# Performance work log

Measured on AMD Instinct MI355X. Metric: run time of the kernel, lower is better.

Reference implementation:

```python
import jax, jax.numpy as jnp
import numpy as np

S, B, I, H = 2048, 64, 256, 512


def setup_inputs() -> dict:
    key = jax.random.key(0)
    ks = jax.random.split(key, 13)
    f = lambda k, sh: jax.random.normal(k, sh, dtype=jnp.float32) * 0.05
    m = lambda k, sh: jax.random.randint(k, sh, 0, 2, dtype=jnp.int32)
    return {
        "x": f(ks[0], (S, B, I)),
        "W_ih0": f(ks[1], (H, I)),
        "W_hh0": f(ks[2], (H, H)),
        "b_ih0": f(ks[3], (H,)),
        "b_hh0": f(ks[4], (H,)),
        "W_ih1": f(ks[5], (H, H)),
        "W_hh1": f(ks[6], (H, H)),
        "b_ih1": f(ks[7], (H,)),
        "b_hh1": f(ks[8], (H,)),
        "mask_ih0": m(ks[9], (H, I)),
        "mask_hh0": m(ks[10], (H, H)),
        "mask_ih1": m(ks[11], (H, H)),
        "mask_hh1": m(ks[12], (H, H)),
    }


def _rnn_layer(x, Wih, Whh, bih, bhh):
    # x: [S, B, in]; tanh RNN layer, h0 = zeros. Precompute input projection
    # for all timesteps (one big GEMM), then scan the recurrence.
    xb = jnp.einsum('sbi,hi->sbh', x, Wih) + bih + bhh  # [S, B, H]

    def step(h, xt):
        h = jnp.tanh(xt + h @ Whh.T)
        return h, h

    h0 = jnp.zeros((x.shape[1], Whh.shape[0]), dtype=x.dtype)
    _, ys = jax.lax.scan(step, h0, xb)
    return ys  # [S, B, H]


def reference(x, W_ih0, W_hh0, b_ih0, b_hh0, W_ih1, W_hh1, b_ih1, b_hh1,
              mask_ih0, mask_hh0, mask_ih1, mask_hh1):
    dt = x.dtype
    y0 = _rnn_layer(x,
                    W_ih0 * mask_ih0.astype(dt), W_hh0 * mask_hh0.astype(dt),
                    b_ih0, b_hh0)
    y1 = _rnn_layer(y0,
                    W_ih1 * mask_ih1.astype(dt), W_hh1 * mask_hh1.astype(dt),
                    b_ih1, b_hh1)
    return y1[-1]  # last timestep hidden state: [B, H]
```

## Files before the change

### kernel.cpp

```cpp
#include <hip/hip_runtime.h>
#include <math.h>

typedef unsigned int u32;
typedef unsigned long long u64;
typedef unsigned short u16;
typedef __attribute__((ext_vector_type(8))) short short8;
typedef __attribute__((ext_vector_type(4))) float f4;
typedef __attribute__((ext_vector_type(4))) u32 u32x4;

#define Ssz 2048
#define Bsz 64
#define Isz 256
#define Hsz 512
#define KC0 24
#define KC1 32

#define WB0_OFF   0u
#define WB1_OFF   1572864u
#define BIAS0_OFF 3670016u
#define BIAS1_OFF 3672064u
#define FLAGS_OFF 3674112u
#define H0_OFF    3675136u
#define H1_OFF    4068352u

#define MFMA(a, b, c) __builtin_amdgcn_mfma_f32_16x16x32_bf16(a, b, c, 0, 0, 0)

__device__ __forceinline__ u16 f2bf(float f) {
  union { float f; u32 u; } v; v.f = f;
  u32 r = v.u + 0x7FFFu + ((v.u >> 16) & 1u);
  return (u16)(r >> 16);
}
__device__ __forceinline__ float bf2f(u16 h) {
  union { u32 u; float f; } v; v.u = ((u32)h) << 16;
  return v.f;
}
__device__ __forceinline__ u32 packbf(float f) {
  u16 hi = f2bf(f);
  u16 lo = f2bf(f - bf2f(hi));
  return (u32)hi | ((u32)lo << 16);
}
__device__ __forceinline__ void unpack2(u32 w0, u32 w1, u32& hi, u32& lo) {
  hi = __builtin_amdgcn_perm(w1, w0, 0x05040100u);
  lo = __builtin_amdgcn_perm(w1, w0, 0x07060302u);
}
__device__ __forceinline__ void cvt2(float a, float b, u32& hi, u32& lo) {
  u16 ha = f2bf(a), hb = f2bf(b);
  u16 la = f2bf(a - bf2f(ha)), lb = f2bf(b - bf2f(hb));
  hi = (u32)ha | ((u32)hb << 16);
  lo = (u32)la | ((u32)lb << 16);
}
__device__ __forceinline__ float ftanh(float xx) {
  float x = fminf(20.f, fmaxf(-20.f, xx));
  float e = __expf(2.f * x);
  return (e - 1.f) / (e + 1.f);
}

union frag { short8 s; u32 w[4]; };

__device__ __forceinline__ u64 ald64(const u64* p) {
  return __hip_atomic_load(p, __ATOMIC_RELAXED, __HIP_MEMORY_SCOPE_AGENT);
}
__device__ __forceinline__ u32 ald32(const u32* p) {
  return __hip_atomic_load(p, __ATOMIC_RELAXED, __HIP_MEMORY_SCOPE_AGENT);
}
__device__ __forceinline__ void ast32(u32* p, u32 v) {
  __hip_atomic_store(p, v, __ATOMIC_RELAXED, __HIP_MEMORY_SCOPE_AGENT);
}

__device__ __forceinline__ void spin_load(const u32* rb, int ks, int lane,
                                          u32 tag, u64 (&hb)[8][4]) {
  const u64 M = 0x0001000000010000ull;
  const u64 E = tag ? M : 0ull;
  while (1) {
    #pragma unroll
    for (int i = 0; i < 8; ++i) {
      const u64* pp = (const u64*)(rb + (2 * i + ks) * 512 + lane * 8);
      #pragma unroll
      for (int v = 0; v < 4; ++v) hb[i][v] = ald64(pp + v);
    }
    int ok = 1;
    #pragma unroll
    for (int i = 0; i < 8; ++i)
      #pragma unroll
      for (int v = 0; v < 4; ++v) ok &= (int)((hb[i][v] & M) == E);
    if (__all(ok)) break;
  }
}

__global__ void prep_weights(const float* __restrict__ Wih0, const float* __restrict__ Whh0,
                             const float* __restrict__ bih0, const float* __restrict__ bhh0,
                             const float* __restrict__ Wih1, const float* __restrict__ Whh1,
                             const float* __restrict__ bih1, const float* __restrict__ bhh1,
                             const int* __restrict__ mih0, const int* __restrict__ mhh0,
                             const int* __restrict__ mih1, const int* __restrict__ mhh1,
                             char* __restrict__ ws) {
  const int L0E = 768 * 512, L1E = 1024 * 512;
  const int TAGN = 3 * 32768;
  int e = blockIdx.x * blockDim.x + threadIdx.x;
  if (e >= L0E + L1E + 1024 + TAGN) return;
  if (e < L0E) {
    int f = e >> 9, fe = e & 511;
    int lane = fe >> 3, j = fe & 7;
    int n = lane & 15, q = lane >> 4;
    int nt = f / KC0, kc = f % KC0;
    int u = nt * 16 + n, k = kc * 32 + q * 8 + j;
    float w;
    if (k < 256) w = Wih0[u * 256 + k] * (float)mih0[u * 256 + k];
    else         w = Whh0[u * 512 + (k - 256)] * (float)mhh0[u * 512 + (k - 256)];
    ((u32*)(ws + WB0_OFF))[e] = packbf(w);
  } else if (e < L0E + L1E) {
    int e1 = e - L0E;
    int f = e1 >> 9, fe = e1 & 511;
    int lane = fe >> 3, j = fe & 7;
    int n = lane & 15, q = lane >> 4;
    int nt = f >> 5, kc = f & 31;
    int u = nt * 16 + n, k = kc * 32 + q * 8 + j;
    float w;
    if (k < 512) w = Wih1[u * 512 + k] * (float)mih1[u * 512 + k];
    else         w = Whh1[u * 512 + (k - 512)] * (float)mhh1[u * 512 + (k - 512)];
    ((u32*)(ws + WB1_OFF))[e1] = packbf(w);
  } else if (e < L0E + L1E + 1024) {
    int b2 = e - L0E - L1E;
    if (b2 < 512) ((float*)(ws + BIAS0_OFF))[b2] = bih0[b2] + bhh0[b2];
    else          ((float*)(ws + BIAS1_OFF))[b2 - 512] = bih1[b2 - 512] + bhh1[b2 - 512];
  } else {
    int ti = e - (L0E + L1E + 1024);
    u32* dst;
    if (ti < 32768)      dst = (u32*)(ws + H0_OFF) + ti;
    else if (ti < 65536) dst = (u32*)(ws + H0_OFF) + 32768 + ti;
    else                 dst = (u32*)(ws + H1_OFF) + (ti - 65536);
    *dst = 0x00010000u;
  }
}


__device__ __forceinline__ void run0(const float* __restrict__ x, char* __restrict__ ws,
                                     int m, int p, int tid, float (*red)[256]) {
  const int w = tid >> 6, lane = tid & 63, n = lane & 15, q = lane >> 4;
  const int nt = p * 4 + (w & 3), ks = w >> 2;
  const int b0 = m * 16;
  const u32* WB = (const u32*)(ws + WB0_OFF);
  u32* flags1 = (u32*)(ws + FLAGS_OFF + m * 256) + 16;
  const float bs = ((const float*)(ws + BIAS0_OFF))[nt * 16 + n];

  short8 Whi[12], Wlo[12];
  #pragma unroll
  for (int i = 0; i < 12; ++i) {
    const int kcg = 2 * i + ks;
    const u32* pw = WB + ((nt * KC0 + kcg) * 64 + lane) * 8;
    u32x4 a = *(const u32x4*)pw;
    u32x4 b = *(const u32x4*)(pw + 4);
    frag h, l;
    unpack2(a.x, a.y, h.w[0], l.w[0]);
    unpack2(a.z, a.w, h.w[1], l.w[1]);
    unpack2(b.x, b.y, h.w[2], l.w[2]);
    unpack2(b.z, b.w, h.w[3], l.w[3]);
    Whi[i] = h.s; Wlo[i] = l.s;
  }

  f4 xp[4][2];
  auto loadx = [&](int t) {
    #pragma unroll
    for (int i = 0; i < 4; ++i) {
      const int kcg = 2 * i + ks;
      const float* sx = x + ((long)t * Bsz + b0 + n) * Isz + kcg * 32 + q * 8;
      xp[i][0] = *(const f4*)sx;
      xp[i][1] = *(const f4*)(sx + 4);
    }
  };
  short8 Axh[4], Axl[4];
  auto cvtx = [&]() {
    #pragma unroll
    for (int i = 0; i < 4; ++i) {
      frag h, l;
      #pragma unroll
      for (int v = 0; v < 2; ++v) {
        f4 f = xp[i][v];
        cvt2(f.x, f.y, h.w[2 * v], l.w[2 * v]);
        cvt2(f.z, f.w, h.w[2 * v + 1], l.w[2 * v + 1]);
      }
      Axh[i] = h.s; Axl[i] = l.s;
    }
  };
  loadx(0); cvtx();

  const int cst = (nt * 16 + n) >> 5;
  const int qp = ((nt * 2) + (n >> 3)) & 3;
  const int jj = n & 7;
  int last1 = 0;

  for (int t = 0; t < Ssz; ++t) {
    f4 acc0 = {0.f, 0.f, 0.f, 0.f}, acc1 = {0.f, 0.f, 0.f, 0.f};
    #pragma unroll
    for (int i = 0; i < 4; ++i) {
      acc0 = MFMA(Axh[i], Whi[i], acc0);
      acc1 = MFMA(Axh[i], Wlo[i], acc1);
      acc0 = MFMA(Axl[i], Whi[i], acc0);
    }
    loadx(t + 1 < Ssz ? t + 1 : t);
    const u32* rb = (const u32*)(ws + H0_OFF) + (((t + 2) % 3) * 4 + m) * 8192;
    u64 hb[8][4];
    spin_load(rb, ks, lane, (u32)((t + 1) & 1), hb);
    #pragma unroll
    for (int i = 0; i < 8; ++i) {
      frag h, l;
      #pragma unroll
      for (int v = 0; v < 4; ++v)
        unpack2((u32)hb[i][v], (u32)(hb[i][v] >> 32), h.w[v], l.w[v]);
      acc0 = MFMA(h.s, Whi[4 + i], acc0);
      acc1 = MFMA(h.s, Wlo[4 + i], acc1);
      acc0 = MFMA(l.s, Whi[4 + i], acc0);
    }
    f4 acc = acc0 + acc1;
    if (tid == 0 && last1 < t - 2) {
      const int tgt = t - 2;
      while (1) {
        int mn = 0x7fffffff;
        #pragma unroll
        for (int i = 0; i < 8; ++i) { int f = (int)ald32(flags1 + i); if (f < mn) mn = f; }
        if (mn >= tgt) { last1 = mn; break; }
      }
    }
    *(f4*)&red[w][lane * 4] = acc;
    __syncthreads();
    if (w < 4) {
      u32* wb = (u32*)(ws + H0_OFF) + ((t % 3) * 4 + m) * 8192;
      const u32 tb = (u32)(t & 1) << 16;
      f4 s0 = *(f4*)&red[w][lane * 4];
      f4 s1 = *(f4*)&red[w + 4][lane * 4];
      #pragma unroll
      for (int r = 0; r < 4; ++r) {
        float val = ftanh(bs + s0[r] + s1[r]);
        u32 pv = (packbf(val) & 0xFFFEFFFFu) | tb;
        ast32(wb + cst * 512 + ((q * 4 + r) + 16 * qp) * 8 + jj, pv);
      }
    }
    __syncthreads();
    cvtx();
  }
}

__device__ __forceinline__ void run1(char* __restrict__ ws, float* __restrict__ out,
                                     int m, int p, int tid, float (*red)[256]) {
  const int w = tid >> 6, lane = tid & 63, n = lane & 15, q = lane >> 4;
  const int nt = p * 4 + (w & 3), ks = w >> 2;
  const int b0 = m * 16;
  const u32* WB = (const u32*)(ws + WB1_OFF);
  u32* flags1 = (u32*)(ws + FLAGS_OFF + m * 256) + 16;
  const float bs = ((const float*)(ws + BIAS1_OFF))[nt * 16 + n];

  short8 Whi[16], Wlo[16];
  #pragma unroll
  for (int i = 0; i < 16; ++i) {
    const int kcg = 2 * i + ks;
    const u32* pw = WB + ((nt * KC1 + kcg) * 64 + lane) * 8;
    u32x4 a = *(const u32x4*)pw;
    u32x4 b = *(const u32x4*)(pw + 4);
    frag h, l;
    unpack2(a.x, a.y, h.w[0], l.w[0]);
    unpack2(a.z, a.w, h.w[1], l.w[1]);
    unpack2(b.x, b.y, h.w[2], l.w[2]);
    unpack2(b.z, b.w, h.w[3], l.w[3]);
    Whi[i] = h.s; Wlo[i] = l.s;
  }

  const int cst = (nt * 16 + n) >> 5;
  const int qp = ((nt * 2) + (n >> 3)) & 3;
  const int jj = n & 7;

  for (int t = 1; t <= Ssz; ++t) {
    f4 acc0 = {0.f, 0.f, 0.f, 0.f}, acc1 = {0.f, 0.f, 0.f, 0.f};
    {
      const u32* rb = (const u32*)(ws + H0_OFF) + (((t - 1) % 3) * 4 + m) * 8192;
      u64 hb[8][4];
      spin_load(rb, ks, lane, (u32)((t - 1) & 1), hb);
      #pragma unroll
      for (int i = 0; i < 8; ++i) {
        frag h, l;
        #pragma unroll
        for (int v = 0; v < 4; ++v)
          unpack2((u32)hb[i][v], (u32)(hb[i][v] >> 32), h.w[v], l.w[v]);
        acc0 = MFMA(h.s, Whi[i], acc0);
        acc1 = MFMA(h.s, Wlo[i], acc1);
        acc0 = MFMA(l.s, Whi[i], acc0);
      }
    }
    {
      const u32* rb = (const u32*)(ws + H1_OFF) + ((t & 1) * 4 + m) * 8192;
      u64 hb[8][4];
      spin_load(rb, ks, lane, (u32)(((t - 1) >> 1) & 1), hb);
      #pragma unroll
      for (int i = 0; i < 8; ++i) {
        frag h, l;
        #pragma unroll
        for (int v = 0; v < 4; ++v)
          unpack2((u32)hb[i][v], (u32)(hb[i][v] >> 32), h.w[v], l.w[v]);
        acc0 = MFMA(h.s, Whi[8 + i], acc0);
        acc1 = MFMA(h.s, Wlo[8 + i], acc1);
        acc0 = MFMA(l.s, Whi[8 + i], acc0);
      }
    }
    f4 acc = acc0 + acc1;
    *(f4*)&red[w][lane * 4] = acc;
    __syncthreads();
    if (tid == 0) ast32(flags1 + p, (u32)t);
    if (w < 4) {
      u32* wb = (u32*)(ws + H1_OFF) + (((t - 1) & 1) * 4 + m) * 8192;
      const u32 tb = (u32)((t >> 1) & 1) << 16;
      f4 s0 = *(f4*)&red[w][lane * 4];
      f4 s1 = *(f4*)&red[w + 4][lane * 4];
      #pragma unroll
      for (int r = 0; r < 4; ++r) {
        float val = ftanh(bs + s0[r] + s1[r]);
        u32 pv = (packbf(val) & 0xFFFEFFFFu) | tb;
        ast32(wb + cst * 512 + ((q * 4 + r) + 16 * qp) * 8 + jj, pv);
        if (t == Ssz) out[(b0 + q * 4 + r) * Hsz + nt * 16 + n] = val;
      }
    }
    __syncthreads();
  }
}

__global__ __launch_bounds__(512, 2) void rnn_persist(const float* __restrict__ x,
                                                      char* __restrict__ ws,
                                                      float* __restrict__ out) {
  __shared__ float red[8][256];
  const int tid = threadIdx.x;
  const int wg = blockIdx.x;
  const int m = (wg >> 3) & 3, p = wg & 7;
  if (wg < 32) run0(x, ws, m, p, tid, red);
  else         run1(ws, out, m, p, tid, red);
}

extern "C" void kernel_launch(void* const* d_in, const int* in_sizes, int n_in,
                              void* d_out, int out_size, void* d_ws, size_t ws_size,
                              hipStream_t stream) {
  const float* x    = (const float*)d_in[0];
  const float* Wih0 = (const float*)d_in[1];
  const float* Whh0 = (const float*)d_in[2];
  const float* bih0 = (const float*)d_in[3];
  const float* bhh0 = (const float*)d_in[4];
  const float* Wih1 = (const float*)d_in[5];
  const float* Whh1 = (const float*)d_in[6];
  const float* bih1 = (const float*)d_in[7];
  const float* bhh1 = (const float*)d_in[8];
  const int* mih0   = (const int*)d_in[9];
  const int* mhh0   = (const int*)d_in[10];
  const int* mih1   = (const int*)d_in[11];
  const int* mhh1   = (const int*)d_in[12];
  char* ws = (char*)d_ws;

  hipMemsetAsync(ws + FLAGS_OFF, 0, 1024 + 393216 + 262144, stream);

  const int tot = 768 * 512 + 1024 * 512 + 1024 + 3 * 32768;
  prep_weights<<<(tot + 255) / 256, 256, 0, stream>>>(
      Wih0, Whh0, bih0, bhh0, Wih1, Whh1, bih1, bhh1,
      mih0, mhh0, mih1, mhh1, ws);

  rnn_persist<<<64, 512, 0, stream>>>(x, ws, (float*)d_out);
}
```

Measured before the change: 16.10 ms.

## Drop intra-block K-split reduction; one wave owns full K per tile with deeper ring

Each wave now computes a full 16-wide output tile over the whole K dimension, keeping all weight fragments in registers. This removes the shared-memory reduction and both __syncthreads per timestep, and blocks shrink to 256 threads. The hidden-state ring buffers deepen (5 slots for layer 0, 3 for layer 1), so layer 0 can run further ahead before waiting on per-wave layer-1 flags. Each wave also uses four independent MFMA accumulators to break the dependency chain. The cost is doubled register pressure per wave and serial spin loads of the full hidden state per wave, with half as many waves to hide latency.

```diff
diff --git a/kernel.cpp b/kernel.cpp
--- a/kernel.cpp
+++ b/kernel.cpp
@@ -14,6 +14,8 @@
 #define Hsz 512
 #define KC0 24
 #define KC1 32
+#define D0 5
+#define D1 3
 
 #define WB0_OFF   0u
 #define WB1_OFF   1572864u
@@ -21,7 +23,7 @@
 #define BIAS1_OFF 3672064u
 #define FLAGS_OFF 3674112u
 #define H0_OFF    3675136u
-#define H1_OFF    4068352u
+#define H1_OFF    4330496u
 
 #define MFMA(a, b, c) __builtin_amdgcn_mfma_f32_16x16x32_bf16(a, b, c, 0, 0, 0)
 
@@ -67,16 +69,16 @@
   __hip_atomic_store(p, v, __ATOMIC_RELAXED, __HIP_MEMORY_SCOPE_AGENT);
 }
 
-__device__ __forceinline__ void spin_load(const u32* rb, int ks, int lane,
-                                          u32 tag, u64 (&hb)[8][4]) {
+__device__ __forceinline__ void spin8(const u32* rb, int cbase, int lane,
+                                      u32 par, u64 (&hb)[8][4]) {
   const u64 M = 0x0001000000010000ull;
-  const u64 E = tag ? M : 0ull;
+  const u64 E = par ? M : 0ull;
+  const u64* base = (const u64*)(rb + cbase * 512 + lane * 8);
   while (1) {
     #pragma unroll
     for (int i = 0; i < 8; ++i) {
-      const u64* pp = (const u64*)(rb + (2 * i + ks) * 512 + lane * 8);
       #pragma unroll
-      for (int v = 0; v < 4; ++v) hb[i][v] = ald64(pp + v);
+      for (int v = 0; v < 4; ++v) hb[i][v] = ald64(base + i * 256 + v);
     }
     int ok = 1;
     #pragma unroll
@@ -86,6 +88,16 @@
     if (__all(ok)) break;
   }
 }
+
+#define HSTEP(ii, WH, WL) do { frag h_, l_;                                 \
+    unpack2((u32)hb[ii][0], (u32)(hb[ii][0] >> 32), h_.w[0], l_.w[0]);      \
+    unpack2((u32)hb[ii][1], (u32)(hb[ii][1] >> 32), h_.w[1], l_.w[1]);      \
+    unpack2((u32)hb[ii][2], (u32)(hb[ii][2] >> 32), h_.w[2], l_.w[2]);      \
+    unpack2((u32)hb[ii][3], (u32)(hb[ii][3] >> 32), h_.w[3], l_.w[3]);      \
+    c[(ii) & 3]       = MFMA(h_.s, WH, c[(ii) & 3]);                        \
+    c[((ii) + 1) & 3] = MFMA(h_.s, WL, c[((ii) + 1) & 3]);                  \
+    c[((ii) + 2) & 3] = MFMA(l_.s, WH, c[((ii) + 2) & 3]);                  \
+  } while (0)
 
 __global__ void prep_weights(const float* __restrict__ Wih0, const float* __restrict__ Whh0,
                              const float* __restrict__ bih0, const float* __restrict__ bhh0,
@@ -95,7 +107,7 @@
                              const int* __restrict__ mih1, const int* __restrict__ mhh1,
                              char* __restrict__ ws) {
   const int L0E = 768 * 512, L1E = 1024 * 512;
-  const int TAGN = 3 * 32768;
+  const int TAGN = 131072;
   int e = blockIdx.x * blockDim.x + threadIdx.x;
   if (e >= L0E + L1E + 1024 + TAGN) return;
   if (e < L0E) {
@@ -126,28 +138,29 @@
   } else {
     int ti = e - (L0E + L1E + 1024);
     u32* dst;
-    if (ti < 32768)      dst = (u32*)(ws + H0_OFF) + ti;
-    else if (ti < 65536) dst = (u32*)(ws + H0_OFF) + 32768 + ti;
-    else                 dst = (u32*)(ws + H1_OFF) + (ti - 65536);
+    if (ti < 98304) {
+      int s = ti >> 15;
+      dst = (u32*)(ws + H0_OFF) + (2 * s) * 32768 + (ti & 32767);
+    } else {
+      dst = (u32*)(ws + H1_OFF) + 2 * 32768 + (ti - 98304);
+    }
     *dst = 0x00010000u;
   }
 }
 
 
 __device__ __forceinline__ void run0(const float* __restrict__ x, char* __restrict__ ws,
-                                     int m, int p, int tid, float (*red)[256]) {
-  const int w = tid >> 6, lane = tid & 63, n = lane & 15, q = lane >> 4;
-  const int nt = p * 4 + (w & 3), ks = w >> 2;
+                                     int m, int nt, int lane) {
+  const int n = lane & 15, q = lane >> 4;
   const int b0 = m * 16;
   const u32* WB = (const u32*)(ws + WB0_OFF);
-  u32* flags1 = (u32*)(ws + FLAGS_OFF + m * 256) + 16;
   const float bs = ((const float*)(ws + BIAS0_OFF))[nt * 16 + n];
-
-  short8 Whi[12], Wlo[12];
+  const u32* fl = (const u32*)(ws + FLAGS_OFF) + m * 64;
+
+  short8 Whi[KC0], Wlo[KC0];
   #pragma unroll
-  for (int i = 0; i < 12; ++i) {
-    const int kcg = 2 * i + ks;
-    const u32* pw = WB + ((nt * KC0 + kcg) * 64 + lane) * 8;
+  for (int kc = 0; kc < KC0; ++kc) {
+    const u32* pw = WB + ((nt * KC0 + kc) * 64 + lane) * 8;
     u32x4 a = *(const u32x4*)pw;
     u32x4 b = *(const u32x4*)(pw + 4);
     frag h, l;
@@ -155,105 +168,87 @@
     unpack2(a.z, a.w, h.w[1], l.w[1]);
     unpack2(b.x, b.y, h.w[2], l.w[2]);
     unpack2(b.z, b.w, h.w[3], l.w[3]);
-    Whi[i] = h.s; Wlo[i] = l.s;
-  }
-
-  f4 xp[4][2];
+    Whi[kc] = h.s; Wlo[kc] = l.s;
+  }
+
+  f4 xp[8][2];
   auto loadx = [&](int t) {
     #pragma unroll
-    for (int i = 0; i < 4; ++i) {
-      const int kcg = 2 * i + ks;
-      const float* sx = x + ((long)t * Bsz + b0 + n) * Isz + kcg * 32 + q * 8;
+    for (int i = 0; i < 8; ++i) {
+      const float* sx = x + ((long)t * Bsz + b0 + n) * Isz + i * 32 + q * 8;
       xp[i][0] = *(const f4*)sx;
       xp[i][1] = *(const f4*)(sx + 4);
     }
   };
-  short8 Axh[4], Axl[4];
+  short8 Axh[8], Axl[8];
   auto cvtx = [&]() {
     #pragma unroll
-    for (int i = 0; i < 4; ++i) {
+    for (int i = 0; i < 8; ++i) {
       frag h, l;
-      #pragma unroll
-      for (int v = 0; v < 2; ++v) {
-        f4 f = xp[i][v];
-        cvt2(f.x, f.y, h.w[2 * v], l.w[2 * v]);
-        cvt2(f.z, f.w, h.w[2 * v + 1], l.w[2 * v + 1]);
-      }
+      cvt2(xp[i][0].x, xp[i][0].y, h.w[0], l.w[0]);
+      cvt2(xp[i][0].z, xp[i][0].w, h.w[1], l.w[1]);
+      cvt2(xp[i][1].x, xp[i][1].y, h.w[2], l.w[2]);
+      cvt2(xp[i][1].z, xp[i][1].w, h.w[3], l.w[3]);
       Axh[i] = h.s; Axl[i] = l.s;
     }
   };
   loadx(0); cvtx();
 
-  const int cst = (nt * 16 + n) >> 5;
-  const int qp = ((nt * 2) + (n >> 3)) & 3;
-  const int jj = n & 7;
-  int last1 = 0;
+  const int sbase = (nt >> 1) * 512 +
+                    (q * 4 + 16 * (((nt & 1) << 1) + (n >> 3))) * 8 + (n & 7);
+  int sR = D0 - 1, sW = 0, last1 = 0;
+  u64 hb[8][4];
 
   for (int t = 0; t < Ssz; ++t) {
-    f4 acc0 = {0.f, 0.f, 0.f, 0.f}, acc1 = {0.f, 0.f, 0.f, 0.f};
-    #pragma unroll
-    for (int i = 0; i < 4; ++i) {
-      acc0 = MFMA(Axh[i], Whi[i], acc0);
-      acc1 = MFMA(Axh[i], Wlo[i], acc1);
-      acc0 = MFMA(Axl[i], Whi[i], acc0);
+    f4 c[4] = {{0,0,0,0},{0,0,0,0},{0,0,0,0},{0,0,0,0}};
+    #pragma unroll
+    for (int i = 0; i < 8; ++i) {
+      c[i & 3]       = MFMA(Axh[i], Whi[i], c[i & 3]);
+      c[(i + 1) & 3] = MFMA(Axh[i], Wlo[i], c[(i + 1) & 3]);
+      c[(i + 2) & 3] = MFMA(Axl[i], Whi[i], c[(i + 2) & 3]);
     }
     loadx(t + 1 < Ssz ? t + 1 : t);
-    const u32* rb = (const u32*)(ws + H0_OFF) + (((t + 2) % 3) * 4 + m) * 8192;
-    u64 hb[8][4];
-    spin_load(rb, ks, lane, (u32)((t + 1) & 1), hb);
-    #pragma unroll
-    for (int i = 0; i < 8; ++i) {
-      frag h, l;
-      #pragma unroll
-      for (int v = 0; v < 4; ++v)
-        unpack2((u32)hb[i][v], (u32)(hb[i][v] >> 32), h.w[v], l.w[v]);
-      acc0 = MFMA(h.s, Whi[4 + i], acc0);
-      acc1 = MFMA(h.s, Wlo[4 + i], acc1);
-      acc0 = MFMA(l.s, Whi[4 + i], acc0);
-    }
-    f4 acc = acc0 + acc1;
-    if (tid == 0 && last1 < t - 2) {
-      const int tgt = t - 2;
+    const u32 pr = (u32)((t - 1) & 1);
+    const u32* rb = (const u32*)(ws + H0_OFF) + (sR * 4 + m) * 8192;
+    spin8(rb, 0, lane, pr, hb);
+    #pragma unroll
+    for (int i = 0; i < 8; ++i) HSTEP(i, Whi[8 + i], Wlo[8 + i]);
+    spin8(rb, 8, lane, pr, hb);
+    #pragma unroll
+    for (int i = 0; i < 8; ++i) HSTEP(i, Whi[16 + i], Wlo[16 + i]);
+    f4 s = (c[0] + c[1]) + (c[2] + c[3]);
+    if (last1 < t - 4) {
       while (1) {
-        int mn = 0x7fffffff;
+        int mn = 1 << 30;
         #pragma unroll
-        for (int i = 0; i < 8; ++i) { int f = (int)ald32(flags1 + i); if (f < mn) mn = f; }
-        if (mn >= tgt) { last1 = mn; break; }
+        for (int i = 0; i < 32; ++i) { int f = (int)ald32(fl + i); mn = f < mn ? f : mn; }
+        if (mn >= t - 4) { last1 = mn; break; }
       }
     }
-    *(f4*)&red[w][lane * 4] = acc;
-    __syncthreads();
-    if (w < 4) {
-      u32* wb = (u32*)(ws + H0_OFF) + ((t % 3) * 4 + m) * 8192;
-      const u32 tb = (u32)(t & 1) << 16;
-      f4 s0 = *(f4*)&red[w][lane * 4];
-      f4 s1 = *(f4*)&red[w + 4][lane * 4];
-      #pragma unroll
-      for (int r = 0; r < 4; ++r) {
-        float val = ftanh(bs + s0[r] + s1[r]);
-        u32 pv = (packbf(val) & 0xFFFEFFFFu) | tb;
-        ast32(wb + cst * 512 + ((q * 4 + r) + 16 * qp) * 8 + jj, pv);
-      }
-    }
-    __syncthreads();
+    u32* wb = (u32*)(ws + H0_OFF) + (sW * 4 + m) * 8192;
+    const u32 tb = (u32)(t & 1) << 16;
+    #pragma unroll
+    for (int r = 0; r < 4; ++r) {
+      float val = ftanh(bs + s[r]);
+      ast32(wb + sbase + r * 8, (packbf(val) & 0xFFFEFFFFu) | tb);
+    }
+    sR = (sR == D0 - 1) ? 0 : sR + 1;
+    sW = (sW == D0 - 1) ? 0 : sW + 1;
     cvtx();
   }
 }
 
 __device__ __forceinline__ void run1(char* __restrict__ ws, float* __restrict__ out,
-                                     int m, int p, int tid, float (*red)[256]) {
-  const int w = tid >> 6, lane = tid & 63, n = lane & 15, q = lane >> 4;
-  const int nt = p * 4 + (w & 3), ks = w >> 2;
-  const int b0 = m * 16;
+                                     int m, int nt, int lane) {
+  const int n = lane & 15, q = lane >> 4;
   const u32* WB = (const u32*)(ws + WB1_OFF);
-  u32* flags1 = (u32*)(ws + FLAGS_OFF + m * 256) + 16;
   const float bs = ((const float*)(ws + BIAS1_OFF))[nt * 16 + n];
-
-  short8 Whi[16], Wlo[16];
+  u32* myflag = (u32*)(ws + FLAGS_OFF) + m * 64 + nt;
+
+  short8 Whi[KC1], Wlo[KC1];
   #pragma unroll
-  for (int i = 0; i < 16; ++i) {
-    const int kcg = 2 * i + ks;
-    const u32* pw = WB + ((nt * KC1 + kcg) * 64 + lane) * 8;
+  for (int kc = 0; kc < KC1; ++kc) {
+    const u32* pw = WB + ((nt * KC1 + kc) * 64 + lane) * 8;
     u32x4 a = *(const u32x4*)pw;
     u32x4 b = *(const u32x4*)(pw + 4);
     frag h, l;
@@ -261,75 +256,59 @@
     unpack2(a.z, a.w, h.w[1], l.w[1]);
     unpack2(b.x, b.y, h.w[2], l.w[2]);
     unpack2(b.z, b.w, h.w[3], l.w[3]);
-    Whi[i] = h.s; Wlo[i] = l.s;
-  }
-
-  const int cst = (nt * 16 + n) >> 5;
-  const int qp = ((nt * 2) + (n >> 3)) & 3;
-  const int jj = n & 7;
+    Whi[kc] = h.s; Wlo[kc] = l.s;
+  }
+
+  const int sbase = (nt >> 1) * 512 +
+                    (q * 4 + 16 * (((nt & 1) << 1) + (n >> 3))) * 8 + (n & 7);
+  int sR0 = 0, sR1 = 0, sW1 = 1;
+  u64 hb[8][4];
 
   for (int t = 1; t <= Ssz; ++t) {
-    f4 acc0 = {0.f, 0.f, 0.f, 0.f}, acc1 = {0.f, 0.f, 0.f, 0.f};
-    {
-      const u32* rb = (const u32*)(ws + H0_OFF) + (((t - 1) % 3) * 4 + m) * 8192;
-      u64 hb[8][4];
-      spin_load(rb, ks, lane, (u32)((t - 1) & 1), hb);
-      #pragma unroll
-      for (int i = 0; i < 8; ++i) {
-        frag h, l;
-        #pragma unroll
-        for (int v = 0; v < 4; ++v)
-          unpack2((u32)hb[i][v], (u32)(hb[i][v] >> 32), h.w[v], l.w[v]);
-        acc0 = MFMA(h.s, Whi[i], acc0);
-        acc1 = MFMA(h.s, Wlo[i], acc1);
-        acc0 = MFMA(l.s, Whi[i], acc0);
-      }
-    }
-    {
-      const u32* rb = (const u32*)(ws + H1_OFF) + ((t & 1) * 4 + m) * 8192;
-      u64 hb[8][4];
-      spin_load(rb, ks, lane, (u32)(((t - 1) >> 1) & 1), hb);
-      #pragma unroll
-      for (int i = 0; i < 8; ++i) {
-        frag h, l;
-        #pragma unroll
-        for (int v = 0; v < 4; ++v)
-          unpack2((u32)hb[i][v], (u32)(hb[i][v] >> 32), h.w[v], l.w[v]);
-        acc0 = MFMA(h.s, Whi[8 + i], acc0);
-        acc1 = MFMA(h.s, Wlo[8 + i], acc1);
-        acc0 = MFMA(l.s, Whi[8 + i], acc0);
-      }
-    }
-    f4 acc = acc0 + acc1;
-    *(f4*)&red[w][lane * 4] = acc;
-    __syncthreads();
-    if (tid == 0) ast32(flags1 + p, (u32)t);
-    if (w < 4) {
-      u32* wb = (u32*)(ws + H1_OFF) + (((t - 1) & 1) * 4 + m) * 8192;
-      const u32 tb = (u32)((t >> 1) & 1) << 16;
-      f4 s0 = *(f4*)&red[w][lane * 4];
-      f4 s1 = *(f4*)&red[w + 4][lane * 4];
-      #pragma unroll
-      for (int r = 0; r < 4; ++r) {
-        float val = ftanh(bs + s0[r] + s1[r]);
-        u32 pv = (packbf(val) & 0xFFFEFFFFu) | tb;
-        ast32(wb + cst * 512 + ((q * 4 + r) + 16 * qp) * 8 + jj, pv);
-        if (t == Ssz) out[(b0 + q * 4 + r) * Hsz + nt * 16 + n] = val;
-      }
-    }
-    __syncthreads();
-  }
-}
-
-__global__ __launch_bounds__(512, 2) void rnn_persist(const float* __restrict__ x,
+    f4 c[4] = {{0,0,0,0},{0,0,0,0},{0,0,0,0},{0,0,0,0}};
+    const u32 pr = (u32)((t - 1) & 1);
+    const u32* rb0 = (const u32*)(ws + H0_OFF) + (sR0 * 4 + m) * 8192;
+    spin8(rb0, 0, lane, pr, hb);
+    #pragma unroll
+    for (int i = 0; i < 8; ++i) HSTEP(i, Whi[i], Wlo[i]);
+    spin8(rb0, 8, lane, pr, hb);
+    #pragma unroll
+    for (int i = 0; i < 8; ++i) HSTEP(i, Whi[8 + i], Wlo[8 + i]);
+    if (lane == 0) ast32(myflag, (u32)t);
+    const u32* rb1 = (const u32*)(ws + H1_OFF) + (sR1 * 4 + m) * 8192;
+    spin8(rb1, 0, lane, pr, hb);
+    #pragma unroll
+    for (int i = 0; i < 8; ++i) HSTEP(i, Whi[16 + i], Wlo[16 + i]);
+    spin8(rb1, 8, lane, pr, hb);
+    #pragma unroll
+    for (int i = 0; i < 8; ++i) HSTEP(i, Whi[24 + i], Wlo[24 + i]);
+    f4 s = (c[0] + c[1]) + (c[2] + c[3]);
+    u32* wb = (u32*)(ws + H1_OFF) + (sW1 * 4 + m) * 8192;
+    const u32 tb = (u32)(t & 1) << 16;
+    #pragma unroll
+    for (int r = 0; r < 4; ++r) {
+      float val = ftanh(bs + s[r]);
+      ast32(wb + sbase + r * 8, (packbf(val) & 0xFFFEFFFFu) | tb);
+      if (t == Ssz) out[(m * 16 + q * 4 + r) * Hsz + nt * 16 + n] = val;
+    }
+    sR0 = (sR0 == D0 - 1) ? 0 : sR0 + 1;
+    sR1 = (sR1 == D1 - 1) ? 0 : sR1 + 1;
+    sW1 = (sW1 == D1 - 1) ? 0 : sW1 + 1;
+  }
+}
+
+__global__ __launch_bounds__(256, 1) void rnn_persist(const float* __restrict__ x,
                                                       char* __restrict__ ws,
                                                       float* __restrict__ out) {
-  __shared__ float red[8][256];
   const int tid = threadIdx.x;
+  const int w = tid >> 6, lane = tid & 63;
   const int wg = blockIdx.x;
-  const int m = (wg >> 3) & 3, p = wg & 7;
-  if (wg < 32) run0(x, ws, m, p, tid, red);
-  else         run1(ws, out, m, p, tid, red);
+  if (wg < 32) {
+    run0(x, ws, wg >> 3, (wg & 7) * 4 + w, lane);
+  } else {
+    const int g = wg - 32;
+    run1(ws, out, g >> 3, (g & 7) * 4 + w, lane);
+  }
 }
 
 extern "C" void kernel_launch(void* const* d_in, const int* in_sizes, int n_in,
@@ -350,12 +329,12 @@
   const int* mhh1   = (const int*)d_in[12];
   char* ws = (char*)d_ws;
 
-  hipMemsetAsync(ws + FLAGS_OFF, 0, 1024 + 393216 + 262144, stream);
-
-  const int tot = 768 * 512 + 1024 * 512 + 1024 + 3 * 32768;
+  hipMemsetAsync(ws + FLAGS_OFF, 0, 1024 + 655360 + 393216, stream);
+
+  const int tot = 768 * 512 + 1024 * 512 + 1024 + 131072;
   prep_weights<<<(tot + 255) / 256, 256, 0, stream>>>(
       Wih0, Whh0, bih0, bhh0, Wih1, Whh1, bih1, bhh1,
       mih0, mhh0, mih1, mhh1, ws);
 
-  rnn_persist<<<64, 512, 0, stream>>>(x, ws, (float*)d_out);
-}
+  rnn_persist<<<64, 256, 0, stream>>>(x, ws, (float*)d_out);
+}
```

After: 30.64 ms. 90.3% more time.
